# Optimization experiments

Measured on AMD Instinct MI355X. Metric: run time of the kernel, lower is better.

Reference implementation:

```python
import jax, jax.numpy as jnp
import numpy as np

N, E, D, H, O = 50000, 800000, 128, 256, 64
BN_EPS = 1e-5


def setup_inputs() -> dict:
    key = jax.random.key(0)
    ks = jax.random.split(key, 12)
    x_indices = jnp.arange(N, dtype=jnp.int64) if jax.config.jax_enable_x64 else jnp.arange(N, dtype=jnp.int32)
    ei = jax.random.randint(ks[0], (2, E), 0, N, dtype=jnp.int32)
    s = lambda k, shape, fan: jax.random.normal(k, shape, dtype=jnp.float32) * (1.0 / np.sqrt(fan))
    return {
        "x_indices": x_indices,
        "ei": ei,
        "emb": jax.random.normal(ks[1], (N, D), dtype=jnp.float32),
        "W1": s(ks[2], (D, H), D), "b1": jnp.zeros((H,), jnp.float32),
        "g1": jnp.ones((H,), jnp.float32), "be1": jnp.zeros((H,), jnp.float32),
        "W2": s(ks[3], (H, H), H), "b2": jnp.zeros((H,), jnp.float32),
        "g2": jnp.ones((H,), jnp.float32), "be2": jnp.zeros((H,), jnp.float32),
        "W3": s(ks[4], (H, O), H), "b3": jnp.zeros((O,), jnp.float32),
    }


def reference(x_indices, ei, emb, W1, b1, g1, be1, W2, b2, g2, be2, W3, b3):
    n = emb.shape[0]
    # GCN normalization with self-loops (PyG GCNConv default):
    loop = jnp.arange(n, dtype=ei.dtype)
    row = jnp.concatenate([ei[0], loop])  # source
    col = jnp.concatenate([ei[1], loop])  # target (aggregation index)
    deg = jax.ops.segment_sum(jnp.ones_like(col, dtype=emb.dtype), col, num_segments=n)
    dinv = jnp.where(deg > 0, 1.0 / jnp.sqrt(jnp.maximum(deg, 1.0)), 0.0)
    norm = dinv[row] * dinv[col]  # [E+N]

    def conv(x, W, b):
        xl = x @ W                                   # [N, d_out]
        msg = xl[row] * norm[:, None]                # gather + scale
        return jax.ops.segment_sum(msg, col, num_segments=n) + b  # scatter-add

    def bn(x, g, be):  # batch-stat BatchNorm1d (training-mode stats)
        m = jnp.mean(x, axis=0)
        v = jnp.var(x, axis=0)
        return (x - m) * (g / jnp.sqrt(v + BN_EPS)) + be

    x = emb[x_indices]
    x = jax.nn.relu(bn(conv(x, W1, b1), g1, be1))
    x = jax.nn.relu(bn(conv(x, W2, b2), g2, be2))
    return conv(x, W3, b3)
```

## Files before the change

kernel.cpp:

```cpp
#include <hip/hip_runtime.h>
#include <hip/hip_bf16.h>

#define Dk 128
#define Hk 256
#define Ok 64
#define BN_EPS 1e-5f

typedef __attribute__((ext_vector_type(8))) short short8;
typedef __attribute__((ext_vector_type(4))) float f32x4;

static __device__ __forceinline__ float bf2f(ushort u) {
    union { uint32_t i; float f; } c; c.i = ((uint32_t)u) << 16; return c.f;
}
static __device__ __forceinline__ ushort f2bf(float f) {
    union { float f; uint32_t u; } c; c.f = f;
    return (ushort)((c.u + 0x7fffu + ((c.u >> 16) & 1u)) >> 16);
}

template<int V> __device__ __forceinline__ void loadv(ushort* d, const ushort* s);
template<> __device__ __forceinline__ void loadv<1>(ushort* d, const ushort* s) { d[0] = *s; }
template<> __device__ __forceinline__ void loadv<2>(ushort* d, const ushort* s) { *(ushort2*)d = *(const ushort2*)s; }
template<> __device__ __forceinline__ void loadv<4>(ushort* d, const ushort* s) { *(ushort4*)d = *(const ushort4*)s; }
template<int V> __device__ __forceinline__ void storev(ushort* d, const ushort* s);
template<> __device__ __forceinline__ void storev<1>(ushort* d, const ushort* s) { *d = s[0]; }
template<> __device__ __forceinline__ void storev<2>(ushort* d, const ushort* s) { *(ushort2*)d = *(const ushort2*)s; }
template<> __device__ __forceinline__ void storev<4>(ushort* d, const ushort* s) { *(ushort4*)d = *(const ushort4*)s; }


__global__ void count_kernel(const int* __restrict__ col, int* __restrict__ cnt, int E) {
    int e = blockIdx.x * blockDim.x + threadIdx.x;
    if (e < E) atomicAdd(&cnt[col[e]], 1);
}

__global__ void dinv_bsum_kernel(const int* __restrict__ cnt, float* __restrict__ dinv,
                                 int* __restrict__ fillc, int* __restrict__ bsum, int n) {
    __shared__ int sm[256];
    int i = blockIdx.x * 256 + threadIdx.x;
    int c = (i < n) ? cnt[i] : 0;
    if (i < n) { dinv[i] = rsqrtf((float)c + 1.0f); fillc[i] = 0; }
    sm[threadIdx.x] = c;
    __syncthreads();
    for (int s = 128; s; s >>= 1) {
        if (threadIdx.x < s) sm[threadIdx.x] += sm[threadIdx.x + s];
        __syncthreads();
    }
    if (!threadIdx.x) bsum[blockIdx.x] = sm[0];
}

__global__ void scan_base_kernel(int* __restrict__ bsum, int nb) {
    __shared__ int sm[256];
    int t = threadIdx.x;
    int carry = 0;
    for (int base = 0; base < nb; base += 256) {
        int i = base + t;
        int v = (i < nb) ? bsum[i] : 0;
        sm[t] = v;
        __syncthreads();
        for (int s = 1; s < 256; s <<= 1) {
            int add = (t >= s) ? sm[t - s] : 0;
            __syncthreads();
            sm[t] += add;
            __syncthreads();
        }
        if (i < nb) bsum[i] = carry + sm[t] - v;
        int tot = sm[255];
        __syncthreads();
        carry += tot;
    }
}

__global__ void scan_final_kernel(const int* __restrict__ cnt, const int* __restrict__ bbase,
                                  int* __restrict__ offv, int n) {
    __shared__ int sm[256];
    int t = threadIdx.x, i = blockIdx.x * 256 + t;
    int v = (i < n) ? cnt[i] : 0;
    sm[t] = v;
    __syncthreads();
    for (int s = 1; s < 256; s <<= 1) {
        int add = (t >= s) ? sm[t - s] : 0;
        __syncthreads();
        sm[t] += add;
        __syncthreads();
    }
    if (i < n) offv[i + 1] = bbase[blockIdx.x] + sm[t];
    if (i == 0) offv[0] = 0;
}

__global__ void fill_kernel(const int* __restrict__ row, const int* __restrict__ col,
                            const int* __restrict__ off, int* __restrict__ fillc,
                            const float* __restrict__ dinv, int2* __restrict__ ep, int E) {
    int e = blockIdx.x * blockDim.x + threadIdx.x;
    if (e < E) {
        int c = col[e], r = row[e];
        int p = atomicAdd(&fillc[c], 1);
        ep[off[c] + p] = make_int2(r, __float_as_int(dinv[r]));
    }
}


__global__ void emb_cvt_kernel(const float* __restrict__ emb, const int* __restrict__ xidx,
                               ushort* __restrict__ out, int n) {
    int gid = blockIdx.x * 256 + threadIdx.x;
    int total = n * (Dk / 8);
    if (gid >= total) return;
    int node = gid >> 4, seg = gid & 15;
    int src = xidx[node];
    const float* p = &emb[(size_t)src * Dk + seg * 8];
    float4 lo = *(const float4*)p, hi = *(const float4*)(p + 4);
    ushort r[8] = {f2bf(lo.x), f2bf(lo.y), f2bf(lo.z), f2bf(lo.w),
                   f2bf(hi.x), f2bf(hi.y), f2bf(hi.z), f2bf(hi.w)};
    *(short8*)&out[(size_t)gid * 8] = *(short8*)r;
}

#define W1SZ (Dk * Hk)
#define W2SZ (Hk * Hk)
#define W3SZ (Hk * Ok)
#define WBLK ((W1SZ + W2SZ + W3SZ) / 256)
#define STATSP_FLOATS (2 * 64 * 512)
__global__ void wcvt_all_kernel(const float* __restrict__ W1, const float* __restrict__ W2,
                                const float* __restrict__ W3, ushort* __restrict__ W1t,
                                ushort* __restrict__ W2t, ushort* __restrict__ W3t,
                                float* __restrict__ statsP) {
    int bid = blockIdx.x;
    if (bid >= WBLK) {
        int idx = (bid - WBLK) * 1024 + threadIdx.x * 4;
        if (idx < STATSP_FLOATS)
            *(float4*)&statsP[idx] = make_float4(0.f, 0.f, 0.f, 0.f);
        return;
    }
    int gid = bid * 256 + threadIdx.x;
    if (gid < W1SZ) {
        int c = gid / Dk, k = gid - c * Dk;
        W1t[gid] = f2bf(W1[(size_t)k * Hk + c]);
    } else if (gid < W1SZ + W2SZ) {
        int idx = gid - W1SZ;
        int c = idx / Hk, k = idx - c * Hk;
        W2t[idx] = f2bf(W2[(size_t)k * Hk + c]);
    } else {
        int idx = gid - W1SZ - W2SZ;
        int c = idx / Hk, k = idx - c * Hk;
        W3t[idx] = f2bf(W3[(size_t)k * Ok + c]);
    }
}

__global__ void bn_finalize_kernel(const float* __restrict__ statsP, const float* __restrict__ g,
                                   const float* __restrict__ be, float* __restrict__ ss,
                                   float invn) {
    int f = threadIdx.x;
    float sum = 0.f, sq = 0.f;
    for (int s = 0; s < 64; ++s) {
        sum += statsP[s * 512 + f];
        sq  += statsP[s * 512 + 256 + f];
    }
    float mean = sum * invn;
    float var = sq * invn - mean * mean;
    float sc = g[f] * rsqrtf(var + BN_EPS);
    ss[f] = sc;
    ss[256 + f] = fmaf(-mean, sc, be[f]);
}


template<int KD, int BNT, bool STATS, bool BIAS, bool BN_A>
__global__ __launch_bounds__(256) void gemm128(
    const ushort* __restrict__ A, const ushort* __restrict__ Wt,
    ushort* __restrict__ Cout, int n, int Hout,
    const float* __restrict__ bias, float* __restrict__ statsP,
    const float* __restrict__ ss)
{
    constexpr int WN = (BNT == 128) ? 2 : 1;
    constexpr int MR = (BNT == 128) ? 4 : 2;
    constexpr int NR = 4;
    constexpr int TILE = (128 + BNT) * 32;
    constexpr int NT = KD / 32;
    __shared__ ushort lds[2 * TILE];
    __shared__ float ssc[BN_A ? KD : 1];
    __shared__ float ssh[BN_A ? KD : 1];

    const int tid = threadIdx.x;
    const int lane = tid & 63, wid = tid >> 6;
    const int wr = wid / WN, wc = wid % WN;
    const int lr = lane & 15, lg = lane >> 4;
    const int bm = blockIdx.x * 128;
    const int bn = blockIdx.y * BNT;

    if (BN_A) {
        for (int f = tid; f < KD; f += 256) {
            ssc[f] = ss[f];
            ssh[f] = ss[KD + f];
        }
        __syncthreads();
    }

    auto stage = [&](int buf, int k0) {
        ushort* As = lds + buf * TILE;
        ushort* Bs = As + 128 * 32;
        #pragma unroll
        for (int c = 0; c < 2; ++c) {
            int boff = wid * 2048 + c * 1024 + lane * 16;
            int row = boff >> 6;
            int k8 = (boff >> 4) & 3;
            int grow = bm + row; if (grow >= n) grow = n - 1;
            const ushort* src = &A[(size_t)grow * KD + k0 + k8 * 8];
            if (BN_A) {
                short8 av = *(const short8*)src;
                ushort r[8];
                #pragma unroll
                for (int j = 0; j < 8; ++j) {
                    int kf = k0 + k8 * 8 + j;
                    float v = bf2f((ushort)av[j]);
                    r[j] = f2bf(fmaxf(fmaf(v, ssc[kf], ssh[kf]), 0.f));
                }
                *(short8*)&As[row * 32 + k8 * 8] = *(short8*)r;
            } else {
                __builtin_amdgcn_global_load_lds(
                    (const __attribute__((address_space(1))) void*)src,
                    (__attribute__((address_space(3))) void*)&As[(wid * 2048 + c * 1024) >> 1],
                    16, 0, 0);
            }
        }
        constexpr int BC = BNT * 64 / 4096;
        #pragma unroll
        for (int c = 0; c < BC; ++c) {
            int boff = wid * (BNT * 16) + c * 1024 + lane * 16;
            int col = boff >> 6;
            int k8 = (boff >> 4) & 3;
            const ushort* src = &Wt[(size_t)(bn + col) * KD + k0 + k8 * 8];
            __builtin_amdgcn_global_load_lds(
                (const __attribute__((address_space(1))) void*)src,
                (__attribute__((address_space(3))) void*)&Bs[(wid * (BNT * 16) + c * 1024) >> 1],
                16, 0, 0);
        }
    };

    f32x4 acc[MR][NR] = {};

    stage(0, 0);
    __syncthreads();
    int cur = 0;
    for (int t = 0; t < NT; ++t) {
        if (t + 1 < NT) stage(cur ^ 1, (t + 1) * 32);
        ushort* As = lds + cur * TILE;
        ushort* Bs = As + 128 * 32;
        short8 af[MR], bfr[NR];
        #pragma unroll
        for (int m = 0; m < MR; ++m)
            af[m] = *(const short8*)&As[(wr * MR * 16 + m * 16 + lr) * 32 + lg * 8];
        #pragma unroll
        for (int nn = 0; nn < NR; ++nn)
            bfr[nn] = *(const short8*)&Bs[(wc * NR * 16 + nn * 16 + lr) * 32 + lg * 8];
        #pragma unroll
        for (int m = 0; m < MR; ++m)
            #pragma unroll
            for (int nn = 0; nn < NR; ++nn)
                acc[m][nn] = __builtin_amdgcn_mfma_f32_16x16x32_bf16(af[m], bfr[nn], acc[m][nn], 0, 0, 0);
        __syncthreads();
        cur ^= 1;
    }

    float s[NR], q[NR];
    #pragma unroll
    for (int nn = 0; nn < NR; ++nn) { s[nn] = 0.f; q[nn] = 0.f; }
    #pragma unroll
    for (int nn = 0; nn < NR; ++nn) {
        int col = bn + wc * NR * 16 + nn * 16 + lr;
        float bv = BIAS ? bias[col] : 0.f;
        #pragma unroll
        for (int m = 0; m < MR; ++m) {
            #pragma unroll
            for (int i = 0; i < 4; ++i) {
                int row = bm + wr * MR * 16 + m * 16 + lg * 4 + i;
                if (row < n) {
                    float v = acc[m][nn][i] + bv;
                    Cout[(size_t)row * Hout + col] = f2bf(v);
                    if (STATS) { s[nn] += v; q[nn] += v * v; }
                }
            }
        }
    }
    if (STATS) {
        float* sp = statsP + (size_t)(blockIdx.x & 63) * 512;
        #pragma unroll
        for (int nn = 0; nn < NR; ++nn) {
            s[nn] += __shfl_xor(s[nn], 16);
            q[nn] += __shfl_xor(q[nn], 16);
            s[nn] += __shfl_xor(s[nn], 32);
            q[nn] += __shfl_xor(q[nn], 32);
            if (lg == 0) {
                int col = bn + wc * NR * 16 + nn * 16 + lr;
                atomicAdd(&sp[col], s[nn]);
                atomicAdd(&sp[256 + col], q[nn]);
            }
        }
    }
}


template<int FH, int MODE>
__global__ __launch_bounds__(256) void agg_kernel(
    const ushort* __restrict__ x, const int2* __restrict__ ep, const int* __restrict__ off,
    const float* __restrict__ dinv, const float* __restrict__ ss,
    const float* __restrict__ bias, void* __restrict__ outp, int n)
{
    constexpr int VEC = FH / 64;
    const int lane = threadIdx.x & 63;
    const int wid = __builtin_amdgcn_readfirstlane(threadIdx.x >> 6);
    const int node = blockIdx.x * 4 + wid;
    if (node >= n) return;
    const int fb = lane * VEC;
    const ushort* __restrict__ xb = x + fb;

    float sc[VEC], sh[VEC];
    if (MODE == 1) {
        #pragma unroll
        for (int v = 0; v < VEC; ++v) { sc[v] = ss[fb + v]; sh[v] = ss[FH + fb + v]; }
    }
    auto xform = [&](ushort u, int v) -> float {
        float val = bf2f(u);
        if (MODE == 1) val = fmaxf(fmaf(val, sc[v], sh[v]), 0.f);
        return val;
    };

    float di = dinv[node];
    float acc[VEC];
    {
        ushort t[VEC];
        loadv<VEC>(t, &xb[(size_t)node * FH]);
        #pragma unroll
        for (int v = 0; v < VEC; ++v) acc[v] = di * xform(t[v], v);
    }
    const int e1 = off[node + 1];
    int e = off[node];
    for (; e + 8 <= e1; e += 8) {
        int2 p[8];
        ushort t[8][VEC];
        #pragma unroll
        for (int j = 0; j < 8; ++j) p[j] = ep[e + j];
        #pragma unroll
        for (int j = 0; j < 8; ++j) loadv<VEC>(t[j], &xb[(size_t)p[j].x * FH]);
        #pragma unroll
        for (int j = 0; j < 8; ++j) {
            float w = __int_as_float(p[j].y);
            #pragma unroll
            for (int v = 0; v < VEC; ++v) acc[v] = fmaf(w, xform(t[j][v], v), acc[v]);
        }
    }
    for (; e + 2 <= e1; e += 2) {
        int2 p0 = ep[e], p1 = ep[e + 1];
        ushort t0[VEC], t1[VEC];
        loadv<VEC>(t0, &xb[(size_t)p0.x * FH]);
        loadv<VEC>(t1, &xb[(size_t)p1.x * FH]);
        float w0 = __int_as_float(p0.y), w1 = __int_as_float(p1.y);
        #pragma unroll
        for (int v = 0; v < VEC; ++v) {
            acc[v] = fmaf(w0, xform(t0[v], v), acc[v]);
            acc[v] = fmaf(w1, xform(t1[v], v), acc[v]);
        }
    }
    if (e < e1) {
        int2 pp = ep[e];
        ushort tt[VEC];
        loadv<VEC>(tt, &xb[(size_t)pp.x * FH]);
        float w = __int_as_float(pp.y);
        #pragma unroll
        for (int v = 0; v < VEC; ++v) acc[v] = fmaf(w, xform(tt[v], v), acc[v]);
    }
    if (MODE == 2) {
        float* o = (float*)outp + (size_t)node * FH + fb;
        #pragma unroll
        for (int v = 0; v < VEC; ++v) o[v] = fmaf(di, acc[v], bias[fb + v]);
    } else {
        ushort ov[VEC];
        #pragma unroll
        for (int v = 0; v < VEC; ++v) ov[v] = f2bf(di * acc[v]);
        storev<VEC>((ushort*)outp + (size_t)node * FH + fb, ov);
    }
}


extern "C" void kernel_launch(void* const* d_in, const int* in_sizes, int n_in,
                              void* d_out, int out_size, void* d_ws, size_t ws_size,
                              hipStream_t stream) {
    const int*   x_idx = (const int*)d_in[0];
    const int*   ei    = (const int*)d_in[1];
    const float* emb   = (const float*)d_in[2];
    const float* W1    = (const float*)d_in[3];
    const float* b1    = (const float*)d_in[4];
    const float* g1    = (const float*)d_in[5];
    const float* be1   = (const float*)d_in[6];
    const float* W2    = (const float*)d_in[7];
    const float* b2    = (const float*)d_in[8];
    const float* g2    = (const float*)d_in[9];
    const float* be2   = (const float*)d_in[10];
    const float* W3    = (const float*)d_in[11];
    const float* b3    = (const float*)d_in[12];

    const int N = in_sizes[0];
    const int E = in_sizes[1] / 2;
    const int* erow = ei;
    const int* ecol = ei + E;

    char* p = (char*)d_ws;
    auto alloc = [&](size_t bytes) { char* q = p; p += (bytes + 255) & ~(size_t)255; return q; };
    const int nb = (N + 255) / 256;
    float*  dinv  = (float*) alloc((size_t)N * 4);
    int*    cnt   = (int*)   alloc((size_t)N * 4);
    int*    off   = (int*)   alloc((size_t)(N + 1) * 4);
    int*    fillc = (int*)   alloc((size_t)N * 4);
    int*    bsum  = (int*)   alloc((size_t)nb * 4);
    int2*   ep    = (int2*)  alloc((size_t)E * 8);
    float*  statsP= (float*) alloc((size_t)STATSP_FLOATS * 4);
    float*  stats1P = statsP, *stats2P = statsP + 64 * 512;
    float*  ss1   = (float*) alloc(512 * 4);
    float*  ss2   = (float*) alloc(512 * 4);
    ushort* W1t   = (ushort*)alloc((size_t)Dk * Hk * 2);
    ushort* W2t   = (ushort*)alloc((size_t)Hk * Hk * 2);
    ushort* W3t   = (ushort*)alloc((size_t)Hk * Ok * 2);
    ushort* bufU  = (ushort*)alloc((size_t)N * Hk * 2);
    ushort* embb  = bufU;
    ushort* agg1b = bufU + (size_t)N * Dk;
    ushort* conv2b= bufU;
    ushort* conv1b= (ushort*)alloc((size_t)N * Hk * 2);
    ushort* agg2b = (ushort*)alloc((size_t)N * Hk * 2);
    ushort* xl3b  = (ushort*)alloc((size_t)N * Ok * 2);

    const float invn = 1.0f / (float)N;

    hipMemsetAsync(cnt, 0, (size_t)N * 4, stream);
    count_kernel<<<(E + 255) / 256, 256, 0, stream>>>(ecol, cnt, E);
    dinv_bsum_kernel<<<nb, 256, 0, stream>>>(cnt, dinv, fillc, bsum, N);
    scan_base_kernel<<<1, 256, 0, stream>>>(bsum, nb);
    scan_final_kernel<<<nb, 256, 0, stream>>>(cnt, bsum, off, N);
    fill_kernel<<<(E + 255) / 256, 256, 0, stream>>>(erow, ecol, off, fillc, dinv, ep, E);

    emb_cvt_kernel<<<(N * (Dk / 8) + 255) / 256, 256, 0, stream>>>(emb, x_idx, embb, N);
    wcvt_all_kernel<<<WBLK + (STATSP_FLOATS + 1023) / 1024, 256, 0, stream>>>(
        W1, W2, W3, W1t, W2t, W3t, statsP);

    const int rb128 = (N + 127) / 128;
    const int aggBlocks = (N + 3) / 4;

    agg_kernel<Dk, 0><<<aggBlocks, 256, 0, stream>>>(
        embb, ep, off, dinv, nullptr, nullptr, agg1b, N);
    gemm128<Dk, 128, true, true, false><<<dim3(rb128, Hk / 128), 256, 0, stream>>>(
        agg1b, W1t, conv1b, N, Hk, b1, stats1P, nullptr);
    bn_finalize_kernel<<<1, 256, 0, stream>>>(stats1P, g1, be1, ss1, invn);

    agg_kernel<Hk, 1><<<aggBlocks, 256, 0, stream>>>(
        conv1b, ep, off, dinv, ss1, nullptr, agg2b, N);
    gemm128<Hk, 128, true, true, false><<<dim3(rb128, Hk / 128), 256, 0, stream>>>(
        agg2b, W2t, conv2b, N, Hk, b2, stats2P, nullptr);
    bn_finalize_kernel<<<1, 256, 0, stream>>>(stats2P, g2, be2, ss2, invn);

    gemm128<Hk, 64, false, false, true><<<dim3(rb128, 1), 256, 0, stream>>>(
        conv2b, W3t, xl3b, N, Ok, nullptr, nullptr, ss2);
    agg_kernel<Ok, 2><<<aggBlocks, 256, 0, stream>>>(
        xl3b, ep, off, dinv, nullptr, b3, d_out, N);
}
```

Baseline: 284.4 us.

## Pack multiple nodes per wavefront in aggregation and merge conversion kernels

The aggregation kernel is parameterized by lanes-per-node so each lane always handles 4 features with 8-byte vector loads. The 128-wide layer now packs 2 nodes per wavefront and the 64-wide layer packs 4, instead of leaving lanes doing 2- or 1-element loads. The embedding conversion, weight conversion and stats zeroing are merged into a single launch to save a kernel launch. Sub-wavefront node groups can diverge when neighbor counts differ, which may cost some lane efficiency.

New measurement: 287.5 us. About the same (+1.1%).

```diff
diff --git a/kernel.cpp b/kernel.cpp
--- a/kernel.cpp
+++ b/kernel.cpp
@@ -16,15 +16,6 @@
     union { float f; uint32_t u; } c; c.f = f;
     return (ushort)((c.u + 0x7fffu + ((c.u >> 16) & 1u)) >> 16);
 }
-
-template<int V> __device__ __forceinline__ void loadv(ushort* d, const ushort* s);
-template<> __device__ __forceinline__ void loadv<1>(ushort* d, const ushort* s) { d[0] = *s; }
-template<> __device__ __forceinline__ void loadv<2>(ushort* d, const ushort* s) { *(ushort2*)d = *(const ushort2*)s; }
-template<> __device__ __forceinline__ void loadv<4>(ushort* d, const ushort* s) { *(ushort4*)d = *(const ushort4*)s; }
-template<int V> __device__ __forceinline__ void storev(ushort* d, const ushort* s);
-template<> __device__ __forceinline__ void storev<1>(ushort* d, const ushort* s) { *d = s[0]; }
-template<> __device__ __forceinline__ void storev<2>(ushort* d, const ushort* s) { *(ushort2*)d = *(const ushort2*)s; }
-template<> __device__ __forceinline__ void storev<4>(ushort* d, const ushort* s) { *(ushort4*)d = *(const ushort4*)s; }
 
 
 __global__ void count_kernel(const int* __restrict__ col, int* __restrict__ cnt, int E) {
@@ -98,49 +89,54 @@
 }
 
 
-__global__ void emb_cvt_kernel(const float* __restrict__ emb, const int* __restrict__ xidx,
-                               ushort* __restrict__ out, int n) {
-    int gid = blockIdx.x * 256 + threadIdx.x;
-    int total = n * (Dk / 8);
-    if (gid >= total) return;
-    int node = gid >> 4, seg = gid & 15;
-    int src = xidx[node];
-    const float* p = &emb[(size_t)src * Dk + seg * 8];
-    float4 lo = *(const float4*)p, hi = *(const float4*)(p + 4);
-    ushort r[8] = {f2bf(lo.x), f2bf(lo.y), f2bf(lo.z), f2bf(lo.w),
-                   f2bf(hi.x), f2bf(hi.y), f2bf(hi.z), f2bf(hi.w)};
-    *(short8*)&out[(size_t)gid * 8] = *(short8*)r;
-}
-
 #define W1SZ (Dk * Hk)
 #define W2SZ (Hk * Hk)
 #define W3SZ (Hk * Ok)
 #define WBLK ((W1SZ + W2SZ + W3SZ) / 256)
 #define STATSP_FLOATS (2 * 64 * 512)
-__global__ void wcvt_all_kernel(const float* __restrict__ W1, const float* __restrict__ W2,
-                                const float* __restrict__ W3, ushort* __restrict__ W1t,
-                                ushort* __restrict__ W2t, ushort* __restrict__ W3t,
-                                float* __restrict__ statsP) {
+
+__global__ void cvt_all_kernel(const float* __restrict__ emb, const int* __restrict__ xidx,
+                               ushort* __restrict__ embb,
+                               const float* __restrict__ W1, const float* __restrict__ W2,
+                               const float* __restrict__ W3, ushort* __restrict__ W1t,
+                               ushort* __restrict__ W2t, ushort* __restrict__ W3t,
+                               float* __restrict__ statsP, int n) {
+    const int embBlocks = (n * (Dk / 8) + 255) >> 8;
     int bid = blockIdx.x;
-    if (bid >= WBLK) {
-        int idx = (bid - WBLK) * 1024 + threadIdx.x * 4;
-        if (idx < STATSP_FLOATS)
-            *(float4*)&statsP[idx] = make_float4(0.f, 0.f, 0.f, 0.f);
+    if (bid < embBlocks) {
+        int gid = bid * 256 + threadIdx.x;
+        int total = n * (Dk / 8);
+        if (gid >= total) return;
+        int node = gid >> 4, seg = gid & 15;
+        int src = xidx[node];
+        const float* p = &emb[(size_t)src * Dk + seg * 8];
+        float4 lo = *(const float4*)p, hi = *(const float4*)(p + 4);
+        ushort r[8] = {f2bf(lo.x), f2bf(lo.y), f2bf(lo.z), f2bf(lo.w),
+                       f2bf(hi.x), f2bf(hi.y), f2bf(hi.z), f2bf(hi.w)};
+        *(short8*)&embb[(size_t)gid * 8] = *(short8*)r;
         return;
     }
-    int gid = bid * 256 + threadIdx.x;
-    if (gid < W1SZ) {
-        int c = gid / Dk, k = gid - c * Dk;
-        W1t[gid] = f2bf(W1[(size_t)k * Hk + c]);
-    } else if (gid < W1SZ + W2SZ) {
-        int idx = gid - W1SZ;
-        int c = idx / Hk, k = idx - c * Hk;
-        W2t[idx] = f2bf(W2[(size_t)k * Hk + c]);
-    } else {
-        int idx = gid - W1SZ - W2SZ;
-        int c = idx / Hk, k = idx - c * Hk;
-        W3t[idx] = f2bf(W3[(size_t)k * Ok + c]);
-    }
+    bid -= embBlocks;
+    if (bid < WBLK) {
+        int gid = bid * 256 + threadIdx.x;
+        if (gid < W1SZ) {
+            int c = gid / Dk, k = gid - c * Dk;
+            W1t[gid] = f2bf(W1[(size_t)k * Hk + c]);
+        } else if (gid < W1SZ + W2SZ) {
+            int idx = gid - W1SZ;
+            int c = idx / Hk, k = idx - c * Hk;
+            W2t[idx] = f2bf(W2[(size_t)k * Hk + c]);
+        } else {
+            int idx = gid - W1SZ - W2SZ;
+            int c = idx / Hk, k = idx - c * Hk;
+            W3t[idx] = f2bf(W3[(size_t)k * Ok + c]);
+        }
+        return;
+    }
+    bid -= WBLK;
+    int idx = bid * 1024 + threadIdx.x * 4;
+    if (idx < STATSP_FLOATS)
+        *(float4*)&statsP[idx] = make_float4(0.f, 0.f, 0.f, 0.f);
 }
 
 __global__ void bn_finalize_kernel(const float* __restrict__ statsP, const float* __restrict__ g,
@@ -295,24 +291,31 @@
 }
 
 
-template<int FH, int MODE>
+template<int FH, int LPN, int MODE>
 __global__ __launch_bounds__(256) void agg_kernel(
     const ushort* __restrict__ x, const int2* __restrict__ ep, const int* __restrict__ off,
     const float* __restrict__ dinv, const float* __restrict__ ss,
     const float* __restrict__ bias, void* __restrict__ outp, int n)
 {
-    constexpr int VEC = FH / 64;
-    const int lane = threadIdx.x & 63;
-    const int wid = __builtin_amdgcn_readfirstlane(threadIdx.x >> 6);
-    const int node = blockIdx.x * 4 + wid;
+    constexpr int VEC = FH / LPN;
+    constexpr int NPW = 64 / LPN;
+    constexpr int NPB = 4 * NPW;
+    const int tid = threadIdx.x;
+    const int lane = tid & 63;
+    const int wid = tid >> 6;
+    const int sub = lane / LPN;
+    const int flane = lane % LPN;
+    const int node = blockIdx.x * NPB + wid * NPW + sub;
     if (node >= n) return;
-    const int fb = lane * VEC;
+    const int fb = flane * VEC;
     const ushort* __restrict__ xb = x + fb;
 
     float sc[VEC], sh[VEC];
     if (MODE == 1) {
-        #pragma unroll
-        for (int v = 0; v < VEC; ++v) { sc[v] = ss[fb + v]; sh[v] = ss[FH + fb + v]; }
+        float4 c4 = *(const float4*)&ss[fb];
+        float4 h4 = *(const float4*)&ss[FH + fb];
+        sc[0] = c4.x; sc[1] = c4.y; sc[2] = c4.z; sc[3] = c4.w;
+        sh[0] = h4.x; sh[1] = h4.y; sh[2] = h4.z; sh[3] = h4.w;
     }
     auto xform = [&](ushort u, int v) -> float {
         float val = bf2f(u);
@@ -323,56 +326,56 @@
     float di = dinv[node];
     float acc[VEC];
     {
-        ushort t[VEC];
-        loadv<VEC>(t, &xb[(size_t)node * FH]);
-        #pragma unroll
-        for (int v = 0; v < VEC; ++v) acc[v] = di * xform(t[v], v);
+        ushort4 t = *(const ushort4*)&xb[(size_t)node * FH];
+        acc[0] = di * xform(t.x, 0); acc[1] = di * xform(t.y, 1);
+        acc[2] = di * xform(t.z, 2); acc[3] = di * xform(t.w, 3);
     }
     const int e1 = off[node + 1];
     int e = off[node];
     for (; e + 8 <= e1; e += 8) {
         int2 p[8];
-        ushort t[8][VEC];
+        ushort4 t[8];
         #pragma unroll
         for (int j = 0; j < 8; ++j) p[j] = ep[e + j];
         #pragma unroll
-        for (int j = 0; j < 8; ++j) loadv<VEC>(t[j], &xb[(size_t)p[j].x * FH]);
+        for (int j = 0; j < 8; ++j) t[j] = *(const ushort4*)&xb[(size_t)p[j].x * FH];
         #pragma unroll
         for (int j = 0; j < 8; ++j) {
             float w = __int_as_float(p[j].y);
-            #pragma unroll
-            for (int v = 0; v < VEC; ++v) acc[v] = fmaf(w, xform(t[j][v], v), acc[v]);
+            acc[0] = fmaf(w, xform(t[j].x, 0), acc[0]);
+            acc[1] = fmaf(w, xform(t[j].y, 1), acc[1]);
+            acc[2] = fmaf(w, xform(t[j].z, 2), acc[2]);
+            acc[3] = fmaf(w, xform(t[j].w, 3), acc[3]);
         }
     }
     for (; e + 2 <= e1; e += 2) {
         int2 p0 = ep[e], p1 = ep[e + 1];
-        ushort t0[VEC], t1[VEC];
-        loadv<VEC>(t0, &xb[(size_t)p0.x * FH]);
-        loadv<VEC>(t1, &xb[(size_t)p1.x * FH]);
+        ushort4 t0 = *(const ushort4*)&xb[(size_t)p0.x * FH];
+        ushort4 t1 = *(const ushort4*)&xb[(size_t)p1.x * FH];
         float w0 = __int_as_float(p0.y), w1 = __int_as_float(p1.y);
-        #pragma unroll
-        for (int v = 0; v < VEC; ++v) {
-            acc[v] = fmaf(w0, xform(t0[v], v), acc[v]);
-            acc[v] = fmaf(w1, xform(t1[v], v), acc[v]);
-        }
+        acc[0] = fmaf(w0, xform(t0.x, 0), acc[0]); acc[1] = fmaf(w0, xform(t0.y, 1), acc[1]);
+        acc[2] = fmaf(w0, xform(t0.z, 2), acc[2]); acc[3] = fmaf(w0, xform(t0.w, 3), acc[3]);
+        acc[0] = fmaf(w1, xform(t1.x, 0), acc[0]); acc[1] = fmaf(w1, xform(t1.y, 1), acc[1]);
+        acc[2] = fmaf(w1, xform(t1.z, 2), acc[2]); acc[3] = fmaf(w1, xform(t1.w, 3), acc[3]);
     }
     if (e < e1) {
         int2 pp = ep[e];
-        ushort tt[VEC];
-        loadv<VEC>(tt, &xb[(size_t)pp.x * FH]);
+        ushort4 tt = *(const ushort4*)&xb[(size_t)pp.x * FH];
         float w = __int_as_float(pp.y);
-        #pragma unroll
-        for (int v = 0; v < VEC; ++v) acc[v] = fmaf(w, xform(tt[v], v), acc[v]);
+        acc[0] = fmaf(w, xform(tt.x, 0), acc[0]); acc[1] = fmaf(w, xform(tt.y, 1), acc[1]);
+        acc[2] = fmaf(w, xform(tt.z, 2), acc[2]); acc[3] = fmaf(w, xform(tt.w, 3), acc[3]);
     }
     if (MODE == 2) {
-        float* o = (float*)outp + (size_t)node * FH + fb;
-        #pragma unroll
-        for (int v = 0; v < VEC; ++v) o[v] = fmaf(di, acc[v], bias[fb + v]);
+        float4 bv = *(const float4*)&bias[fb];
+        float4 res;
+        res.x = fmaf(di, acc[0], bv.x); res.y = fmaf(di, acc[1], bv.y);
+        res.z = fmaf(di, acc[2], bv.z); res.w = fmaf(di, acc[3], bv.w);
+        *(float4*)((float*)outp + (size_t)node * FH + fb) = res;
     } else {
-        ushort ov[VEC];
-        #pragma unroll
-        for (int v = 0; v < VEC; ++v) ov[v] = f2bf(di * acc[v]);
-        storev<VEC>((ushort*)outp + (size_t)node * FH + fb, ov);
+        ushort4 o;
+        o.x = f2bf(di * acc[0]); o.y = f2bf(di * acc[1]);
+        o.z = f2bf(di * acc[2]); o.w = f2bf(di * acc[3]);
+        *(ushort4*)((ushort*)outp + (size_t)node * FH + fb) = o;
     }
 }
 
@@ -432,20 +435,19 @@
     scan_final_kernel<<<nb, 256, 0, stream>>>(cnt, bsum, off, N);
     fill_kernel<<<(E + 255) / 256, 256, 0, stream>>>(erow, ecol, off, fillc, dinv, ep, E);
 
-    emb_cvt_kernel<<<(N * (Dk / 8) + 255) / 256, 256, 0, stream>>>(emb, x_idx, embb, N);
-    wcvt_all_kernel<<<WBLK + (STATSP_FLOATS + 1023) / 1024, 256, 0, stream>>>(
-        W1, W2, W3, W1t, W2t, W3t, statsP);
+    const int embBlocks = (N * (Dk / 8) + 255) / 256;
+    cvt_all_kernel<<<embBlocks + WBLK + (STATSP_FLOATS + 1023) / 1024, 256, 0, stream>>>(
+        emb, x_idx, embb, W1, W2, W3, W1t, W2t, W3t, statsP, N);
 
     const int rb128 = (N + 127) / 128;
-    const int aggBlocks = (N + 3) / 4;
-
-    agg_kernel<Dk, 0><<<aggBlocks, 256, 0, stream>>>(
+
+    agg_kernel<Dk, 32, 0><<<(N + 7) / 8, 256, 0, stream>>>(
         embb, ep, off, dinv, nullptr, nullptr, agg1b, N);
     gemm128<Dk, 128, true, true, false><<<dim3(rb128, Hk / 128), 256, 0, stream>>>(
         agg1b, W1t, conv1b, N, Hk, b1, stats1P, nullptr);
     bn_finalize_kernel<<<1, 256, 0, stream>>>(stats1P, g1, be1, ss1, invn);
 
-    agg_kernel<Hk, 1><<<aggBlocks, 256, 0, stream>>>(
+    agg_kernel<Hk, 64, 1><<<(N + 3) / 4, 256, 0, stream>>>(
         conv1b, ep, off, dinv, ss1, nullptr, agg2b, N);
     gemm128<Hk, 128, true, true, false><<<dim3(rb128, Hk / 128), 256, 0, stream>>>(
         agg2b, W2t, conv2b, N, Hk, b2, stats2P, nullptr);
@@ -453,6 +455,6 @@
 
     gemm128<Hk, 64, false, false, true><<<dim3(rb128, 1), 256, 0, stream>>>(
         conv2b, W3t, xl3b, N, Ok, nullptr, nullptr, ss2);
-    agg_kernel<Ok, 2><<<aggBlocks, 256, 0, stream>>>(
+    agg_kernel<Ok, 16, 2><<<(N + 15) / 16, 256, 0, stream>>>(
         xl3b, ep, off, dinv, nullptr, b3, d_out, N);
 }
```
